# Kernel optimization log

Hardware: AMD Instinct MI355X
Metric: run time of the kernel (lower is better)

## Reference

```python
import jax, jax.numpy as jnp
import numpy as np

N_IM, N_OBJ = 16, 16          # images, objects per image
D_IN = 2048                    # obj_pair_feat_dim
PER_IM = N_OBJ * (N_OBJ + 1) // 2   # obj boxes + union boxes per image
N_BOX = N_IM * PER_IM               # 2176
N_PAIR = N_IM * N_OBJ * (N_OBJ - 1) # is_ex=True -> 2*C(n,2) per image = 3840
NUM_REL = 3


def setup_inputs() -> dict:
    rng = np.random.default_rng(0)
    H, W = 600.0, 800.0
    boxes = np.zeros((N_BOX, 5), np.float32)
    o1i, o2i, ui, imi = [], [], [], []
    for i in range(N_IM):
        off = i * PER_IM
        x1 = rng.uniform(0, W / 2, N_OBJ); y1 = rng.uniform(0, H / 2, N_OBJ)
        bw = rng.uniform(10, W / 2, N_OBJ); bh = rng.uniform(10, H / 2, N_OBJ)
        boxes[off:off + N_OBJ] = np.stack([np.full(N_OBJ, i), x1, y1, x1 + bw, y1 + bh], 1)
        uc = off + N_OBJ
        for a in range(N_OBJ):
            for b in range(a + 1, N_OBJ):
                boxes[uc] = [i, min(x1[a], x1[b]), min(y1[a], y1[b]),
                             max(x1[a] + bw[a], x1[b] + bw[b]), max(y1[a] + bh[a], y1[b] + bh[b])]
                o1i += [off + a, off + b]; o2i += [off + b, off + a]
                ui += [uc, uc]; imi += [i, i]
                uc += 1
    im_info = np.tile(np.array([H, W, 1.0], np.float32), (N_IM, 1))
    key = jax.random.key(0)
    ks = jax.random.split(key, 16)
    lin = lambda k, i, o: jax.random.normal(k, (i, o), jnp.float32) * 0.02
    return dict(
        xs=jax.random.normal(ks[0], (N_PAIR, D_IN), jnp.float32) * 0.1,
        xo=jax.random.normal(ks[1], (N_PAIR, D_IN), jnp.float32) * 0.1,
        xu=jax.random.normal(ks[2], (N_PAIR, D_IN), jnp.float32) * 0.1,
        boxes=jnp.asarray(boxes), im_info=jnp.asarray(im_info),
        o1_idx=jnp.asarray(o1i, jnp.int32), o2_idx=jnp.asarray(o2i, jnp.int32),
        u_idx=jnp.asarray(ui, jnp.int32), img_idx=jnp.asarray(imi, jnp.int32),
        Ws1=lin(ks[3], D_IN, 512), bs1=jnp.zeros(512, jnp.float32),
        Ws2=lin(ks[4], 512, 256), bs2=jnp.zeros(256, jnp.float32),
        Wo1=lin(ks[5], D_IN, 512), bo1=jnp.zeros(512, jnp.float32),
        Wo2=lin(ks[6], 512, 256), bo2=jnp.zeros(256, jnp.float32),
        Wu1=lin(ks[7], D_IN, 512), bu1=jnp.zeros(512, jnp.float32),
        Wu2=lin(ks[8], 512, 256), bu2=jnp.zeros(256, jnp.float32),
        Wc1=lin(ks[9], 256 + 19, 256), bc1=jnp.zeros(256, jnp.float32),
        Wc2=lin(ks[10], 256, NUM_REL), bc2=jnp.zeros(NUM_REL, jnp.float32),
    )


def _mlp(x, W1, b1, W2, b2):
    return jax.nn.relu(jax.nn.relu(x @ W1 + b1) @ W2 + b2)


def _encode_loc(sb, ob, ub, hw):
    # sb/ob/ub: [P,4] (x1,y1,x2,y2); hw: [P,2] (h_i, w_i)
    h_i, w_i = hw[:, 0], hw[:, 1]
    x_s = (sb[:, 0] + sb[:, 2]) / 2.0; y_s = (sb[:, 1] + sb[:, 3]) / 2.0
    w_s = sb[:, 2] - sb[:, 0]; h_s = sb[:, 3] - sb[:, 1]
    x_o = (ob[:, 0] + ob[:, 2]) / 2.0; y_o = (ob[:, 1] + ob[:, 3]) / 2.0
    w_o = ob[:, 2] - ob[:, 0]; h_o = ob[:, 3] - ob[:, 1]
    a_s = w_s * h_s; a_o = w_o * h_o
    a_u = (ub[:, 2] - ub[:, 0]) * (ub[:, 3] - ub[:, 1])
    area = w_i * h_i
    return jnp.stack([
        x_s / w_i, y_s / h_i, (x_s + w_s) / w_i, (y_s + h_s) / h_i, a_s / area,
        x_o / w_i, y_o / h_i, (x_o + w_o) / w_i, (y_o + h_o) / h_i, a_o / area,
        (x_s - x_o) / w_o, (y_s - y_o) / h_o, jnp.log(w_s / w_o), jnp.log(h_s / h_o),
        (x_o - x_s) / w_s, (y_o - y_s) / h_s, jnp.log(w_o / w_s), jnp.log(h_o / h_s),
        a_u / area], axis=1)  # [P,19]


def reference(xs, xo, xu, boxes, im_info, o1_idx, o2_idx, u_idx, img_idx,
              Ws1, bs1, Ws2, bs2, Wo1, bo1, Wo2, bo2, Wu1, bu1, Wu2, bu2,
              Wc1, bc1, Wc2, bc2):
    fs = _mlp(xs, Ws1, bs1, Ws2, bs2)
    fo = _mlp(xo, Wo1, bo1, Wo2, bo2)
    fu = _mlp(xu, Wu1, bu1, Wu2, bu2)
    appear = fu - fo - fs                              # [P,256]
    loc = _encode_loc(boxes[o1_idx, 1:5], boxes[o2_idx, 1:5],
                      boxes[u_idx, 1:5], im_info[img_idx, :2])  # [P,19]
    h = jax.nn.relu(jnp.concatenate([appear, loc], axis=1) @ Wc1 + bc1)
    return h @ Wc2 + bc2                               # [P,num_rel]
```

## Files before the change

### kernel.cpp

```cpp
#include <hip/hip_runtime.h>

#define N_PAIR 3840

typedef short bf16x8 __attribute__((ext_vector_type(8)));
typedef float f32x4 __attribute__((ext_vector_type(4)));

static __device__ __forceinline__ ushort f2bf(float f) {
    uint x = __float_as_uint(f);
    uint r = (x + 0x7FFFu + ((x >> 16) & 1u)) >> 16;
    return (ushort)r;
}
static __device__ __forceinline__ float bf2f(ushort u) {
    return __uint_as_float(((uint)u) << 16);
}

__global__ void transpose_convert(const float* __restrict__ in0,
                                  const float* __restrict__ in1,
                                  const float* __restrict__ in2,
                                  ushort* __restrict__ out,
                                  int K, int N, int Kpad) {
    const float* in = (blockIdx.z == 0) ? in0 : (blockIdx.z == 1 ? in1 : in2);
    ushort* o = out + (size_t)blockIdx.z * N * Kpad;
    __shared__ float tile[64][65];
    int k0 = blockIdx.x * 64, n0 = blockIdx.y * 64;
    int t = threadIdx.x;
    int r = t >> 2, c4 = (t & 3) * 16;
#pragma unroll
    for (int i = 0; i < 16; i++) {
        int k = k0 + r, n = n0 + c4 + i;
        tile[r][c4 + i] = (k < K && n < N) ? in[(size_t)k * N + n] : 0.f;
    }
    __syncthreads();
#pragma unroll
    for (int i = 0; i < 16; i++) {
        int n = n0 + r, k = k0 + c4 + i;
        if (n < N && k < Kpad) o[(size_t)n * Kpad + k] = f2bf(tile[c4 + i][r]);
    }
}

__global__ void transpose_convert2(const float* __restrict__ Ws2,
                                   const float* __restrict__ Wo2,
                                   const float* __restrict__ Wu2,
                                   const float* __restrict__ Wc1,
                                   ushort* __restrict__ W2T,
                                   ushort* __restrict__ WC1T) {
    int z = blockIdx.z;
    const float* in; ushort* o; int K, N, Kpad;
    if (z < 3) {
        in = (z == 0) ? Ws2 : (z == 1 ? Wo2 : Wu2);
        o = W2T + (size_t)z * 256 * 512; K = 512; N = 256; Kpad = 512;
    } else {
        in = Wc1; o = WC1T; K = 275; N = 256; Kpad = 288;
    }
    __shared__ float tile[64][65];
    int k0 = blockIdx.x * 64, n0 = blockIdx.y * 64;
    int t = threadIdx.x;
    int r = t >> 2, c4 = (t & 3) * 16;
#pragma unroll
    for (int i = 0; i < 16; i++) {
        int k = k0 + r, n = n0 + c4 + i;
        tile[r][c4 + i] = (k < K && n < N) ? in[(size_t)k * N + n] : 0.f;
    }
    __syncthreads();
#pragma unroll
    for (int i = 0; i < 16; i++) {
        int n = n0 + r, k = k0 + c4 + i;
        if (n < N && k < Kpad) o[(size_t)n * Kpad + k] = f2bf(tile[c4 + i][r]);
    }
}

__device__ __forceinline__ bf16x8 frag_ld(const ushort* __restrict__ lds, int row, int colbyte) {
    int off = (row << 7) + (colbyte ^ ((row & 7) << 4));
    return *reinterpret_cast<const bf16x8*>(reinterpret_cast<const char*>(lds) + off);
}
__device__ __forceinline__ bf16x8 frag32_ld(const ushort* __restrict__ lds, int row, int colbyte) {
    int off = (row << 6) + (colbyte ^ ((row & 3) << 4));
    return *reinterpret_cast<const bf16x8*>(reinterpret_cast<const char*>(lds) + off);
}

__global__ __launch_bounds__(256) void gemm1(const float* __restrict__ xs,
                                             const float* __restrict__ xo,
                                             const float* __restrict__ xu,
                                             const ushort* __restrict__ w1t,
                                             const float* __restrict__ b_s,
                                             const float* __restrict__ b_o,
                                             const float* __restrict__ b_u,
                                             ushort* __restrict__ h1out) {
    int bid = blockIdx.x;
    int w = (bid & 7) * 90 + (bid >> 3);
    int br = w / 240; int r = w - br * 240;
    int xt = r >> 2, yt = r & 3;

    const float* x = br == 0 ? xs : (br == 1 ? xo : xu);
    const ushort* wt = w1t + (size_t)br * 512 * 2048;
    const float* bias = br == 0 ? b_s : (br == 1 ? b_o : b_u);
    ushort* out = h1out + (size_t)br * 3840 * 512;

    __shared__ ushort As[2][64 * 64];
    __shared__ ushort Bs[2][128 * 64];
    int t = threadIdx.x, lane = t & 63, wid = t >> 6;
    int wr = wid >> 1, wc = wid & 1;
    int m0 = xt * 64, n0 = yt * 128;
    const float* asrc = x + (size_t)m0 * 2048;
    const ushort* bsrc = wt + (size_t)n0 * 2048;

    int ar = t >> 2, ac = (t & 3) * 16;

    float4 pa0[4], pa1[4];
    bf16x8 pb0[4], pb1[4];

#define G1_ISSUE(PA, PB, KT)                                                              \
    {                                                                                     \
        const float4* g = reinterpret_cast<const float4*>(asrc + (size_t)ar * 2048 + (KT) + ac); \
        PA[0] = g[0]; PA[1] = g[1]; PA[2] = g[2]; PA[3] = g[3];                           \
        _Pragma("unroll")                                                                 \
        for (int it = 0; it < 4; it++) {                                                  \
            int e = (it * 256 + t) * 8;                                                   \
            int rr = e >> 6, cc = e & 63;                                                 \
            PB[it] = *reinterpret_cast<const bf16x8*>(bsrc + (size_t)rr * 2048 + (KT) + cc); \
        }                                                                                 \
    }
#define G1_COMMIT(PA, PB, BUF)                                                            \
    {                                                                                     \
        union { bf16x8 v; ushort us[8]; } p0, p1;                                         \
        _Pragma("unroll")                                                                 \
        for (int i = 0; i < 4; i++) {                                                     \
            p0.us[i] = f2bf(PA[0][i]); p0.us[4 + i] = f2bf(PA[1][i]);                     \
            p1.us[i] = f2bf(PA[2][i]); p1.us[4 + i] = f2bf(PA[3][i]);                     \
        }                                                                                 \
        char* ab = reinterpret_cast<char*>(&As[BUF][0]);                                  \
        int off0 = (ar << 7) + ((ac << 1) ^ ((ar & 7) << 4));                             \
        int off1 = (ar << 7) + (((ac + 8) << 1) ^ ((ar & 7) << 4));                       \
        *reinterpret_cast<bf16x8*>(ab + off0) = p0.v;                                     \
        *reinterpret_cast<bf16x8*>(ab + off1) = p1.v;                                     \
        char* bb = reinterpret_cast<char*>(&Bs[BUF][0]);                                  \
        _Pragma("unroll")                                                                 \
        for (int it = 0; it < 4; it++) {                                                  \
            int e = (it * 256 + t) * 8;                                                   \
            int rr = e >> 6, cc = e & 63;                                                 \
            int off = (rr << 7) + ((cc << 1) ^ ((rr & 7) << 4));                          \
            *reinterpret_cast<bf16x8*>(bb + off) = PB[it];                                \
        }                                                                                 \
    }
#define G1_MFMA(BUF)                                                                      \
    _Pragma("unroll")                                                                     \
    for (int kk = 0; kk < 64; kk += 32) {                                                 \
        int cb = (kk + ((lane >> 4) << 3)) << 1;                                          \
        bf16x8 a[2], b[4];                                                                \
        _Pragma("unroll")                                                                 \
        for (int i = 0; i < 2; i++) a[i] = frag_ld(&As[BUF][0], wr * 32 + i * 16 + (lane & 15), cb); \
        _Pragma("unroll")                                                                 \
        for (int f = 0; f < 4; f++) b[f] = frag_ld(&Bs[BUF][0], wc * 64 + f * 16 + (lane & 15), cb); \
        _Pragma("unroll")                                                                 \
        for (int i = 0; i < 2; i++)                                                       \
            _Pragma("unroll")                                                             \
            for (int j = 0; j < 4; j++)                                                   \
                acc[i][j] = __builtin_amdgcn_mfma_f32_16x16x32_bf16(a[i], b[j], acc[i][j], 0, 0, 0); \
    }

    f32x4 acc[2][4] = {};
    G1_ISSUE(pa1, pb1, 0)
    G1_COMMIT(pa1, pb1, 0)
    G1_ISSUE(pa0, pb0, 64)
    __syncthreads();
    for (int kt = 0; kt < 2048; kt += 128) {
        if (kt + 128 < 2048) G1_ISSUE(pa1, pb1, kt + 128)
        G1_MFMA(0)
        if (kt + 64 < 2048) G1_COMMIT(pa0, pb0, 1)
        __syncthreads();
        if (kt + 192 < 2048) G1_ISSUE(pa0, pb0, kt + 192)
        G1_MFMA(1)
        if (kt + 128 < 2048) G1_COMMIT(pa1, pb1, 0)
        __syncthreads();
    }
    int rb = m0 + wr * 32 + ((lane >> 4) << 2);
    int cb0 = n0 + wc * 64 + (lane & 15);
#pragma unroll
    for (int j = 0; j < 4; j++) {
        int col = cb0 + j * 16;
        float bv = bias[col];
#pragma unroll
        for (int i = 0; i < 2; i++)
#pragma unroll
            for (int q = 0; q < 4; q++) {
                int row = rb + i * 16 + q;
                float v = acc[i][j][q] + bv;
                v = v > 0.f ? v : 0.f;
                out[(size_t)row * 512 + col] = f2bf(v);
            }
    }
#undef G1_ISSUE
#undef G1_COMMIT
#undef G1_MFMA
}

__global__ __launch_bounds__(256) void gemm2(const ushort* __restrict__ h1,
                                             const ushort* __restrict__ w2t,
                                             const float* __restrict__ b_s,
                                             const float* __restrict__ b_o,
                                             const float* __restrict__ b_u,
                                             ushort* __restrict__ h2br) {
    int bid = blockIdx.x;
    int w = (bid & 7) * 45 + (bid >> 3);
    int br = w / 120; int r = w - br * 120;
    int xt = r >> 1, yt = r & 1;

    const ushort* A = h1 + (size_t)br * 3840 * 512;
    const ushort* B = w2t + (size_t)br * 256 * 512;
    const float* bias = br == 0 ? b_s : (br == 1 ? b_o : b_u);
    ushort* out = h2br + (size_t)br * 3840 * 256;

    __shared__ ushort As[2][64 * 64];
    __shared__ ushort Bs[2][128 * 64];
    int t = threadIdx.x, lane = t & 63, wid = t >> 6;
    int wr = wid >> 1, wc = wid & 1;
    int m0 = xt * 64, n0 = yt * 128;
    const ushort* asrc = A + (size_t)m0 * 512;
    const ushort* bsrc = B + (size_t)n0 * 512;

    int ar = t >> 2, ac = (t & 3) * 16;
    bf16x8 qa0[2], qa1[2], qb0[4], qb1[4];

#define G2_ISSUE(PA, PB, KT)                                                              \
    {                                                                                     \
        const bf16x8* g = reinterpret_cast<const bf16x8*>(asrc + (size_t)ar * 512 + (KT) + ac); \
        PA[0] = g[0]; PA[1] = g[1];                                                       \
        _Pragma("unroll")                                                                 \
        for (int it = 0; it < 4; it++) {                                                  \
            int e = (it * 256 + t) * 8;                                                   \
            int rr = e >> 6, cc = e & 63;                                                 \
            PB[it] = *reinterpret_cast<const bf16x8*>(bsrc + (size_t)rr * 512 + (KT) + cc); \
        }                                                                                 \
    }
#define G2_COMMIT(PA, PB, BUF)                                                            \
    {                                                                                     \
        char* ab = reinterpret_cast<char*>(&As[BUF][0]);                                  \
        int off0 = (ar << 7) + ((ac << 1) ^ ((ar & 7) << 4));                             \
        int off1 = (ar << 7) + (((ac + 8) << 1) ^ ((ar & 7) << 4));                       \
        *reinterpret_cast<bf16x8*>(ab + off0) = PA[0];                                    \
        *reinterpret_cast<bf16x8*>(ab + off1) = PA[1];                                    \
        char* bb = reinterpret_cast<char*>(&Bs[BUF][0]);                                  \
        _Pragma("unroll")                                                                 \
        for (int it = 0; it < 4; it++) {                                                  \
            int e = (it * 256 + t) * 8;                                                   \
            int rr = e >> 6, cc = e & 63;                                                 \
            int off = (rr << 7) + ((cc << 1) ^ ((rr & 7) << 4));                          \
            *reinterpret_cast<bf16x8*>(bb + off) = PB[it];                                \
        }                                                                                 \
    }
#define G2_MFMA(BUF)                                                                      \
    _Pragma("unroll")                                                                     \
    for (int kk = 0; kk < 64; kk += 32) {                                                 \
        int cb = (kk + ((lane >> 4) << 3)) << 1;                                          \
        bf16x8 a[2], b[4];                                                                \
        _Pragma("unroll")                                                                 \
        for (int i = 0; i < 2; i++) a[i] = frag_ld(&As[BUF][0], wr * 32 + i * 16 + (lane & 15), cb); \
        _Pragma("unroll")                                                                 \
        for (int f = 0; f < 4; f++) b[f] = frag_ld(&Bs[BUF][0], wc * 64 + f * 16 + (lane & 15), cb); \
        _Pragma("unroll")                                                                 \
        for (int i = 0; i < 2; i++)                                                       \
            _Pragma("unroll")                                                             \
            for (int j = 0; j < 4; j++)                                                   \
                acc[i][j] = __builtin_amdgcn_mfma_f32_16x16x32_bf16(a[i], b[j], acc[i][j], 0, 0, 0); \
    }

    f32x4 acc[2][4] = {};
    G2_ISSUE(qa1, qb1, 0)
    G2_COMMIT(qa1, qb1, 0)
    G2_ISSUE(qa0, qb0, 64)
    __syncthreads();
    for (int kt = 0; kt < 512; kt += 128) {
        if (kt + 128 < 512) G2_ISSUE(qa1, qb1, kt + 128)
        G2_MFMA(0)
        if (kt + 64 < 512) G2_COMMIT(qa0, qb0, 1)
        __syncthreads();
        if (kt + 192 < 512) G2_ISSUE(qa0, qb0, kt + 192)
        G2_MFMA(1)
        if (kt + 128 < 512) G2_COMMIT(qa1, qb1, 0)
        __syncthreads();
    }
    int rb = m0 + wr * 32 + ((lane >> 4) << 2);
    int cb0 = n0 + wc * 64 + (lane & 15);
#pragma unroll
    for (int j = 0; j < 4; j++) {
        int col = cb0 + j * 16;
        float bv = bias[col];
#pragma unroll
        for (int i = 0; i < 2; i++)
#pragma unroll
            for (int q = 0; q < 4; q++) {
                int row = rb + i * 16 + q;
                float v = acc[i][j][q] + bv;
                v = v > 0.f ? v : 0.f;
                out[(size_t)row * 256 + col] = f2bf(v);
            }
    }
#undef G2_ISSUE
#undef G2_COMMIT
#undef G2_MFMA
}

__global__ void appear_pack(const ushort* __restrict__ h2br,
                            ushort* __restrict__ hin,
                            const float* __restrict__ boxes,
                            const float* __restrict__ im_info,
                            const int* __restrict__ o1, const int* __restrict__ o2,
                            const int* __restrict__ u, const int* __restrict__ im) {
    int i = blockIdx.x * 256 + threadIdx.x;
    if (i < N_PAIR * 32) {
        int p = i >> 5, ch = (i & 31) * 8;
        const ushort* ps = h2br + (size_t)p * 256 + ch;
        bf16x8 vs = *reinterpret_cast<const bf16x8*>(ps);
        bf16x8 vo = *reinterpret_cast<const bf16x8*>(ps + (size_t)3840 * 256);
        bf16x8 vu = *reinterpret_cast<const bf16x8*>(ps + (size_t)2 * 3840 * 256);
        union { bf16x8 v; ushort us[8]; } r;
#pragma unroll
        for (int j = 0; j < 8; j++)
            r.us[j] = f2bf(bf2f(((ushort)vu[j])) - bf2f(((ushort)vo[j])) - bf2f(((ushort)vs[j])));
        *reinterpret_cast<bf16x8*>(hin + (size_t)p * 288 + ch) = r.v;
    }
    if (blockIdx.x < 15) {
        int p = blockIdx.x * 256 + threadIdx.x;
        const float* sb = boxes + 5 * o1[p] + 1;
        const float* ob = boxes + 5 * o2[p] + 1;
        const float* ub = boxes + 5 * u[p] + 1;
        const float* ii = im_info + 3 * im[p];
        float hi = ii[0], wi = ii[1];
        float x_s = (sb[0] + sb[2]) * 0.5f, y_s = (sb[1] + sb[3]) * 0.5f;
        float w_s = sb[2] - sb[0], h_s = sb[3] - sb[1];
        float x_o = (ob[0] + ob[2]) * 0.5f, y_o = (ob[1] + ob[3]) * 0.5f;
        float w_o = ob[2] - ob[0], h_o = ob[3] - ob[1];
        float a_s = w_s * h_s, a_o = w_o * h_o;
        float a_u = (ub[2] - ub[0]) * (ub[3] - ub[1]);
        float area = wi * hi;
        float f[19];
        f[0] = x_s / wi;            f[1] = y_s / hi;
        f[2] = (x_s + w_s) / wi;    f[3] = (y_s + h_s) / hi;
        f[4] = a_s / area;
        f[5] = x_o / wi;            f[6] = y_o / hi;
        f[7] = (x_o + w_o) / wi;    f[8] = (y_o + h_o) / hi;
        f[9] = a_o / area;
        f[10] = (x_s - x_o) / w_o;  f[11] = (y_s - y_o) / h_o;
        f[12] = logf(w_s / w_o);    f[13] = logf(h_s / h_o);
        f[14] = (x_o - x_s) / w_s;  f[15] = (y_o - y_s) / h_s;
        f[16] = logf(w_o / w_s);    f[17] = logf(h_o / h_s);
        f[18] = a_u / area;
        ushort* row = hin + (size_t)p * 288 + 256;
#pragma unroll
        for (int k = 0; k < 19; k++) row[k] = f2bf(f[k]);
#pragma unroll
        for (int k = 19; k < 32; k++) row[k] = 0;
    }
}

__global__ __launch_bounds__(256) void gemm3(const ushort* __restrict__ hin,
                                             const ushort* __restrict__ wc1t,
                                             const float* __restrict__ bc1,
                                             ushort* __restrict__ h2) {
    __shared__ ushort As[2][64 * 32];
    __shared__ ushort Bs[2][128 * 32];
    int t = threadIdx.x, lane = t & 63, wid = t >> 6;
    int wr = wid >> 1, wc = wid & 1;
    int m0 = blockIdx.x * 64, n0 = blockIdx.y * 128;
    const ushort* asrc = hin + (size_t)m0 * 288;
    const ushort* bsrc = wc1t + (size_t)n0 * 288;

    int ar = t >> 2, ac = (t & 3) * 8;
    bf16x8 pa, pb[2];
    auto issue = [&](int kt) {
        pa = *reinterpret_cast<const bf16x8*>(asrc + (size_t)ar * 288 + kt + ac);
#pragma unroll
        for (int it = 0; it < 2; it++) {
            int e = (it * 256 + t) * 8;
            int rr = e >> 5, cc = e & 31;
            pb[it] = *reinterpret_cast<const bf16x8*>(bsrc + (size_t)rr * 288 + kt + cc);
        }
    };
    auto commit = [&](int buf) {
        char* ab = reinterpret_cast<char*>(&As[buf][0]);
        int off0 = (ar << 6) + ((ac << 1) ^ ((ar & 3) << 4));
        *reinterpret_cast<bf16x8*>(ab + off0) = pa;
        char* bb = reinterpret_cast<char*>(&Bs[buf][0]);
#pragma unroll
        for (int it = 0; it < 2; it++) {
            int e = (it * 256 + t) * 8;
            int rr = e >> 5, cc = e & 31;
            int off = (rr << 6) + ((cc << 1) ^ ((rr & 3) << 4));
            *reinterpret_cast<bf16x8*>(bb + off) = pb[it];
        }
    };

    f32x4 acc[2][4] = {};
    issue(0);
    commit(0);
    __syncthreads();
    int cur = 0;
    for (int kt = 0; kt < 288; kt += 32) {
        int nxt = kt + 32;
        if (nxt < 288) issue(nxt);
        int cb = ((lane >> 4) << 3) << 1;
        bf16x8 a[2], b[4];
#pragma unroll
        for (int i = 0; i < 2; i++) a[i] = frag32_ld(&As[cur][0], wr * 32 + i * 16 + (lane & 15), cb);
#pragma unroll
        for (int f = 0; f < 4; f++) b[f] = frag32_ld(&Bs[cur][0], wc * 64 + f * 16 + (lane & 15), cb);
#pragma unroll
        for (int i = 0; i < 2; i++)
#pragma unroll
            for (int j = 0; j < 4; j++)
                acc[i][j] = __builtin_amdgcn_mfma_f32_16x16x32_bf16(a[i], b[j], acc[i][j], 0, 0, 0);
        if (nxt < 288) commit(cur ^ 1);
        __syncthreads();
        cur ^= 1;
    }
    int rb = m0 + wr * 32 + ((lane >> 4) << 2);
    int cb0 = n0 + wc * 64 + (lane & 15);
#pragma unroll
    for (int j = 0; j < 4; j++) {
        int col = cb0 + j * 16;
        float bv = bc1[col];
#pragma unroll
        for (int i = 0; i < 2; i++)
#pragma unroll
            for (int q = 0; q < 4; q++) {
                int row = rb + i * 16 + q;
                float v = acc[i][j][q] + bv;
                v = v > 0.f ? v : 0.f;
                h2[(size_t)row * 256 + col] = f2bf(v);
            }
    }
}

__global__ void final_fc(const ushort* __restrict__ h2,
                         const float* __restrict__ wc2,
                         const float* __restrict__ bc2,
                         float* __restrict__ out) {
    __shared__ float w[768];
    int t = threadIdx.x;
    for (int i = t; i < 768; i += 256) w[i] = wc2[i];
    __syncthreads();
    int g = t >> 4, l = t & 15;
    int row = blockIdx.x * 16 + g;
    const ushort* hr = h2 + (size_t)row * 256 + l * 16;
    bf16x8 v0 = *reinterpret_cast<const bf16x8*>(hr);
    bf16x8 v1 = *reinterpret_cast<const bf16x8*>(hr + 8);
    float s0 = 0.f, s1 = 0.f, s2 = 0.f;
#pragma unroll
    for (int k = 0; k < 8; k++) {
        float h = bf2f((ushort)v0[k]);
        int c = (l * 16 + k) * 3;
        s0 += h * w[c]; s1 += h * w[c + 1]; s2 += h * w[c + 2];
    }
#pragma unroll
    for (int k = 0; k < 8; k++) {
        float h = bf2f((ushort)v1[k]);
        int c = (l * 16 + 8 + k) * 3;
        s0 += h * w[c]; s1 += h * w[c + 1]; s2 += h * w[c + 2];
    }
#pragma unroll
    for (int m = 1; m < 16; m <<= 1) {
        s0 += __shfl_xor(s0, m);
        s1 += __shfl_xor(s1, m);
        s2 += __shfl_xor(s2, m);
    }
    if (l == 0) {
        out[row * 3 + 0] = s0 + bc2[0];
        out[row * 3 + 1] = s1 + bc2[1];
        out[row * 3 + 2] = s2 + bc2[2];
    }
}

extern "C" void kernel_launch(void* const* d_in, const int* in_sizes, int n_in,
                              void* d_out, int out_size, void* d_ws, size_t ws_size,
                              hipStream_t stream) {
    (void)in_sizes; (void)n_in; (void)out_size; (void)ws_size;
    const float* xs = (const float*)d_in[0];
    const float* xo = (const float*)d_in[1];
    const float* xu = (const float*)d_in[2];
    const float* boxes = (const float*)d_in[3];
    const float* im_info = (const float*)d_in[4];
    const int* o1 = (const int*)d_in[5];
    const int* o2 = (const int*)d_in[6];
    const int* uu = (const int*)d_in[7];
    const int* im = (const int*)d_in[8];
    const float* Ws1 = (const float*)d_in[9];
    const float* bs1 = (const float*)d_in[10];
    const float* Ws2 = (const float*)d_in[11];
    const float* bs2 = (const float*)d_in[12];
    const float* Wo1 = (const float*)d_in[13];
    const float* bo1 = (const float*)d_in[14];
    const float* Wo2 = (const float*)d_in[15];
    const float* bo2 = (const float*)d_in[16];
    const float* Wu1 = (const float*)d_in[17];
    const float* bu1 = (const float*)d_in[18];
    const float* Wu2 = (const float*)d_in[19];
    const float* bu2 = (const float*)d_in[20];
    const float* Wc1 = (const float*)d_in[21];
    const float* bc1 = (const float*)d_in[22];
    const float* Wc2 = (const float*)d_in[23];
    const float* bc2 = (const float*)d_in[24];
    float* out = (float*)d_out;

    ushort* W1T = (ushort*)d_ws;
    ushort* H2BR = W1T;
    ushort* W2T = W1T + (size_t)3 * 512 * 2048;
    ushort* WC1T = W2T + (size_t)3 * 256 * 512;
    ushort* H1 = WC1T + (size_t)256 * 288;
    ushort* HIN = H1 + (size_t)3 * 3840 * 512;
    ushort* H2 = HIN + (size_t)3840 * 288;

    transpose_convert<<<dim3(32, 8, 3), 256, 0, stream>>>(Ws1, Wo1, Wu1, W1T, 2048, 512, 2048);
    transpose_convert2<<<dim3(8, 4, 4), 256, 0, stream>>>(Ws2, Wo2, Wu2, Wc1, W2T, WC1T);
    gemm1<<<720, 256, 0, stream>>>(xs, xo, xu, W1T, bs1, bo1, bu1, H1);
    gemm2<<<360, 256, 0, stream>>>(H1, W2T, bs2, bo2, bu2, H2BR);
    appear_pack<<<480, 256, 0, stream>>>(H2BR, HIN, boxes, im_info, o1, o2, uu, im);
    gemm3<<<dim3(60, 2), 256, 0, stream>>>(HIN, WC1T, bc1, H2);
    final_fc<<<240, 256, 0, stream>>>(H2, Wc2, bc2, out);
}
```

Measured before the change: 97.22 us.

## Retile first-layer GEMM to 128x64 blocks and shorten prefetch distance

```diff
diff --git a/kernel.cpp b/kernel.cpp
--- a/kernel.cpp
+++ b/kernel.cpp
@@ -89,32 +89,33 @@
     int bid = blockIdx.x;
     int w = (bid & 7) * 90 + (bid >> 3);
     int br = w / 240; int r = w - br * 240;
-    int xt = r >> 2, yt = r & 3;
+    int mt = r >> 3, nt = r & 7;
 
     const float* x = br == 0 ? xs : (br == 1 ? xo : xu);
     const ushort* wt = w1t + (size_t)br * 512 * 2048;
     const float* bias = br == 0 ? b_s : (br == 1 ? b_o : b_u);
     ushort* out = h1out + (size_t)br * 3840 * 512;
 
-    __shared__ ushort As[2][64 * 64];
-    __shared__ ushort Bs[2][128 * 64];
+    __shared__ ushort As[2][128 * 64];
+    __shared__ ushort Bs[2][64 * 64];
     int t = threadIdx.x, lane = t & 63, wid = t >> 6;
     int wr = wid >> 1, wc = wid & 1;
-    int m0 = xt * 64, n0 = yt * 128;
+    int m0 = mt * 128, n0 = nt * 64;
     const float* asrc = x + (size_t)m0 * 2048;
     const ushort* bsrc = wt + (size_t)n0 * 2048;
 
-    int ar = t >> 2, ac = (t & 3) * 16;
-
-    float4 pa0[4], pa1[4];
-    bf16x8 pb0[4], pb1[4];
+    int arow = t >> 1, ac0 = (t & 1) * 32;
+
+    float4 pa0[8], pa1[8];
+    bf16x8 pb0[2], pb1[2];
 
 #define G1_ISSUE(PA, PB, KT)                                                              \
     {                                                                                     \
-        const float4* g = reinterpret_cast<const float4*>(asrc + (size_t)ar * 2048 + (KT) + ac); \
-        PA[0] = g[0]; PA[1] = g[1]; PA[2] = g[2]; PA[3] = g[3];                           \
-        _Pragma("unroll")                                                                 \
-        for (int it = 0; it < 4; it++) {                                                  \
+        const float4* g = reinterpret_cast<const float4*>(asrc + (size_t)arow * 2048 + (KT) + ac0); \
+        _Pragma("unroll")                                                                 \
+        for (int i = 0; i < 8; i++) PA[i] = g[i];                                         \
+        _Pragma("unroll")                                                                 \
+        for (int it = 0; it < 2; it++) {                                                  \
             int e = (it * 256 + t) * 8;                                                   \
             int rr = e >> 6, cc = e & 63;                                                 \
             PB[it] = *reinterpret_cast<const bf16x8*>(bsrc + (size_t)rr * 2048 + (KT) + cc); \
@@ -122,20 +123,22 @@
     }
 #define G1_COMMIT(PA, PB, BUF)                                                            \
     {                                                                                     \
-        union { bf16x8 v; ushort us[8]; } p0, p1;                                         \
-        _Pragma("unroll")                                                                 \
-        for (int i = 0; i < 4; i++) {                                                     \
-            p0.us[i] = f2bf(PA[0][i]); p0.us[4 + i] = f2bf(PA[1][i]);                     \
-            p1.us[i] = f2bf(PA[2][i]); p1.us[4 + i] = f2bf(PA[3][i]);                     \
+        char* ab = reinterpret_cast<char*>(&As[BUF][0]);                                  \
+        _Pragma("unroll")                                                                 \
+        for (int j = 0; j < 4; j++) {                                                     \
+            union { bf16x8 v; ushort us[8]; } pk;                                         \
+            _Pragma("unroll")                                                             \
+            for (int i = 0; i < 4; i++) {                                                 \
+                pk.us[i] = f2bf(PA[2 * j][i]);                                            \
+                pk.us[4 + i] = f2bf(PA[2 * j + 1][i]);                                    \
+            }                                                                             \
+            int cj = ac0 + j * 8;                                                         \
+            int off = (arow << 7) + ((cj << 1) ^ ((arow & 7) << 4));                      \
+            *reinterpret_cast<bf16x8*>(ab + off) = pk.v;                                  \
         }                                                                                 \
-        char* ab = reinterpret_cast<char*>(&As[BUF][0]);                                  \
-        int off0 = (ar << 7) + ((ac << 1) ^ ((ar & 7) << 4));                             \
-        int off1 = (ar << 7) + (((ac + 8) << 1) ^ ((ar & 7) << 4));                       \
-        *reinterpret_cast<bf16x8*>(ab + off0) = p0.v;                                     \
-        *reinterpret_cast<bf16x8*>(ab + off1) = p1.v;                                     \
         char* bb = reinterpret_cast<char*>(&Bs[BUF][0]);                                  \
         _Pragma("unroll")                                                                 \
-        for (int it = 0; it < 4; it++) {                                                  \
+        for (int it = 0; it < 2; it++) {                                                  \
             int e = (it * 256 + t) * 8;                                                   \
             int rr = e >> 6, cc = e & 63;                                                 \
             int off = (rr << 7) + ((cc << 1) ^ ((rr & 7) << 4));                          \
@@ -146,41 +149,41 @@
     _Pragma("unroll")                                                                     \
     for (int kk = 0; kk < 64; kk += 32) {                                                 \
         int cb = (kk + ((lane >> 4) << 3)) << 1;                                          \
-        bf16x8 a[2], b[4];                                                                \
-        _Pragma("unroll")                                                                 \
-        for (int i = 0; i < 2; i++) a[i] = frag_ld(&As[BUF][0], wr * 32 + i * 16 + (lane & 15), cb); \
-        _Pragma("unroll")                                                                 \
-        for (int f = 0; f < 4; f++) b[f] = frag_ld(&Bs[BUF][0], wc * 64 + f * 16 + (lane & 15), cb); \
-        _Pragma("unroll")                                                                 \
-        for (int i = 0; i < 2; i++)                                                       \
+        bf16x8 a[4], b[2];                                                                \
+        _Pragma("unroll")                                                                 \
+        for (int i = 0; i < 4; i++) a[i] = frag_ld(&As[BUF][0], wr * 64 + i * 16 + (lane & 15), cb); \
+        _Pragma("unroll")                                                                 \
+        for (int j = 0; j < 2; j++) b[j] = frag_ld(&Bs[BUF][0], wc * 32 + j * 16 + (lane & 15), cb); \
+        _Pragma("unroll")                                                                 \
+        for (int i = 0; i < 4; i++)                                                       \
             _Pragma("unroll")                                                             \
-            for (int j = 0; j < 4; j++)                                                   \
+            for (int j = 0; j < 2; j++)                                                   \
                 acc[i][j] = __builtin_amdgcn_mfma_f32_16x16x32_bf16(a[i], b[j], acc[i][j], 0, 0, 0); \
     }
 
-    f32x4 acc[2][4] = {};
-    G1_ISSUE(pa1, pb1, 0)
-    G1_COMMIT(pa1, pb1, 0)
-    G1_ISSUE(pa0, pb0, 64)
+    f32x4 acc[4][2] = {};
+    G1_ISSUE(pa0, pb0, 0)
+    G1_COMMIT(pa0, pb0, 0)
     __syncthreads();
+    G1_ISSUE(pa1, pb1, 64)
     for (int kt = 0; kt < 2048; kt += 128) {
-        if (kt + 128 < 2048) G1_ISSUE(pa1, pb1, kt + 128)
         G1_MFMA(0)
-        if (kt + 64 < 2048) G1_COMMIT(pa0, pb0, 1)
+        if (kt + 64 < 2048) G1_COMMIT(pa1, pb1, 1)
         __syncthreads();
-        if (kt + 192 < 2048) G1_ISSUE(pa0, pb0, kt + 192)
+        if (kt + 128 < 2048) G1_ISSUE(pa0, pb0, kt + 128)
         G1_MFMA(1)
-        if (kt + 128 < 2048) G1_COMMIT(pa1, pb1, 0)
+        if (kt + 128 < 2048) G1_COMMIT(pa0, pb0, 0)
         __syncthreads();
-    }
-    int rb = m0 + wr * 32 + ((lane >> 4) << 2);
-    int cb0 = n0 + wc * 64 + (lane & 15);
-#pragma unroll
-    for (int j = 0; j < 4; j++) {
+        if (kt + 192 < 2048) G1_ISSUE(pa1, pb1, kt + 192)
+    }
+    int rb = m0 + wr * 64 + ((lane >> 4) << 2);
+    int cb0 = n0 + wc * 32 + (lane & 15);
+#pragma unroll
+    for (int j = 0; j < 2; j++) {
         int col = cb0 + j * 16;
         float bv = bias[col];
 #pragma unroll
-        for (int i = 0; i < 2; i++)
+        for (int i = 0; i < 4; i++)
 #pragma unroll
             for (int q = 0; q < 4; q++) {
                 int row = rb + i * 16 + q;
@@ -265,19 +268,19 @@
     }
 
     f32x4 acc[2][4] = {};
-    G2_ISSUE(qa1, qb1, 0)
-    G2_COMMIT(qa1, qb1, 0)
-    G2_ISSUE(qa0, qb0, 64)
+    G2_ISSUE(qa0, qb0, 0)
+    G2_COMMIT(qa0, qb0, 0)
     __syncthreads();
+    G2_ISSUE(qa1, qb1, 64)
     for (int kt = 0; kt < 512; kt += 128) {
-        if (kt + 128 < 512) G2_ISSUE(qa1, qb1, kt + 128)
         G2_MFMA(0)
-        if (kt + 64 < 512) G2_COMMIT(qa0, qb0, 1)
+        if (kt + 64 < 512) G2_COMMIT(qa1, qb1, 1)
         __syncthreads();
-        if (kt + 192 < 512) G2_ISSUE(qa0, qb0, kt + 192)
+        if (kt + 128 < 512) G2_ISSUE(qa0, qb0, kt + 128)
         G2_MFMA(1)
-        if (kt + 128 < 512) G2_COMMIT(qa1, qb1, 0)
+        if (kt + 128 < 512) G2_COMMIT(qa0, qb0, 0)
         __syncthreads();
+        if (kt + 192 < 512) G2_ISSUE(qa1, qb1, kt + 192)
     }
     int rb = m0 + wr * 32 + ((lane >> 4) << 2);
     int cb0 = n0 + wc * 64 + (lane & 15);
```

After: 161.3 us. 65.9% more time.

## Load bf16 GEMM operands directly into LDS with global_load_lds

Applied to the files above, without the earlier changes.

```diff
diff --git a/kernel.cpp b/kernel.cpp
--- a/kernel.cpp
+++ b/kernel.cpp
@@ -13,6 +13,11 @@
 static __device__ __forceinline__ float bf2f(ushort u) {
     return __uint_as_float(((uint)u) << 16);
 }
+
+#define GLOAD16(GP, LP)                                                        \
+    __builtin_amdgcn_global_load_lds(                                          \
+        (const __attribute__((address_space(1))) void*)(GP),                   \
+        (__attribute__((address_space(3))) void*)(LP), 16, 0, 0)
 
 __global__ void transpose_convert(const float* __restrict__ in0,
                                   const float* __restrict__ in1,
@@ -105,41 +110,36 @@
     const ushort* bsrc = wt + (size_t)n0 * 2048;
 
     int ar = t >> 2, ac = (t & 3) * 16;
-
-    float4 pa0[4], pa1[4];
-    bf16x8 pb0[4], pb1[4];
-
-#define G1_ISSUE(PA, PB, KT)                                                              \
+    float4 pa[4];
+
+#define G1_AISSUE(KT)                                                                     \
     {                                                                                     \
         const float4* g = reinterpret_cast<const float4*>(asrc + (size_t)ar * 2048 + (KT) + ac); \
-        PA[0] = g[0]; PA[1] = g[1]; PA[2] = g[2]; PA[3] = g[3];                           \
-        _Pragma("unroll")                                                                 \
-        for (int it = 0; it < 4; it++) {                                                  \
-            int e = (it * 256 + t) * 8;                                                   \
-            int rr = e >> 6, cc = e & 63;                                                 \
-            PB[it] = *reinterpret_cast<const bf16x8*>(bsrc + (size_t)rr * 2048 + (KT) + cc); \
-        }                                                                                 \
-    }
-#define G1_COMMIT(PA, PB, BUF)                                                            \
+        pa[0] = g[0]; pa[1] = g[1]; pa[2] = g[2]; pa[3] = g[3];                           \
+    }
+#define G1_ACOMMIT(BUF)                                                                   \
     {                                                                                     \
         union { bf16x8 v; ushort us[8]; } p0, p1;                                         \
         _Pragma("unroll")                                                                 \
         for (int i = 0; i < 4; i++) {                                                     \
-            p0.us[i] = f2bf(PA[0][i]); p0.us[4 + i] = f2bf(PA[1][i]);                     \
-            p1.us[i] = f2bf(PA[2][i]); p1.us[4 + i] = f2bf(PA[3][i]);                     \
+            p0.us[i] = f2bf(pa[0][i]); p0.us[4 + i] = f2bf(pa[1][i]);                     \
+            p1.us[i] = f2bf(pa[2][i]); p1.us[4 + i] = f2bf(pa[3][i]);                     \
         }                                                                                 \
         char* ab = reinterpret_cast<char*>(&As[BUF][0]);                                  \
         int off0 = (ar << 7) + ((ac << 1) ^ ((ar & 7) << 4));                             \
         int off1 = (ar << 7) + (((ac + 8) << 1) ^ ((ar & 7) << 4));                       \
         *reinterpret_cast<bf16x8*>(ab + off0) = p0.v;                                     \
         *reinterpret_cast<bf16x8*>(ab + off1) = p1.v;                                     \
-        char* bb = reinterpret_cast<char*>(&Bs[BUF][0]);                                  \
+    }
+#define G1_BGLOAD(BUF, KT)                                                                \
+    {                                                                                     \
         _Pragma("unroll")                                                                 \
         for (int it = 0; it < 4; it++) {                                                  \
-            int e = (it * 256 + t) * 8;                                                   \
-            int rr = e >> 6, cc = e & 63;                                                 \
-            int off = (rr << 7) + ((cc << 1) ^ ((rr & 7) << 4));                          \
-            *reinterpret_cast<bf16x8*>(bb + off) = PB[it];                                \
+            int g = (wid * 4 + it) * 64 + lane;                                           \
+            int rr = g >> 3, cc = g & 7;                                                  \
+            const ushort* gp = bsrc + (size_t)rr * 2048 + (KT) + ((cc ^ (rr & 7)) << 3);  \
+            ushort* lp = &Bs[BUF][g * 8];                                                 \
+            GLOAD16(gp, lp);                                                              \
         }                                                                                 \
     }
 #define G1_MFMA(BUF)                                                                      \
@@ -159,19 +159,20 @@
     }
 
     f32x4 acc[2][4] = {};
-    G1_ISSUE(pa1, pb1, 0)
-    G1_COMMIT(pa1, pb1, 0)
-    G1_ISSUE(pa0, pb0, 64)
+    G1_AISSUE(0)
+    G1_BGLOAD(0, 0)
+    G1_ACOMMIT(0)
     __syncthreads();
-    for (int kt = 0; kt < 2048; kt += 128) {
-        if (kt + 128 < 2048) G1_ISSUE(pa1, pb1, kt + 128)
-        G1_MFMA(0)
-        if (kt + 64 < 2048) G1_COMMIT(pa0, pb0, 1)
+    int cur = 0;
+    for (int kt = 0; kt < 2048; kt += 64) {
+        if (kt + 64 < 2048) {
+            G1_BGLOAD(cur ^ 1, kt + 64)
+            G1_AISSUE(kt + 64)
+        }
+        G1_MFMA(cur)
+        if (kt + 64 < 2048) G1_ACOMMIT(cur ^ 1)
         __syncthreads();
-        if (kt + 192 < 2048) G1_ISSUE(pa0, pb0, kt + 192)
-        G1_MFMA(1)
-        if (kt + 128 < 2048) G1_COMMIT(pa1, pb1, 0)
-        __syncthreads();
+        cur ^= 1;
     }
     int rb = m0 + wr * 32 + ((lane >> 4) << 2);
     int cb0 = n0 + wc * 64 + (lane & 15);
@@ -189,8 +190,9 @@
                 out[(size_t)row * 512 + col] = f2bf(v);
             }
     }
-#undef G1_ISSUE
-#undef G1_COMMIT
+#undef G1_AISSUE
+#undef G1_ACOMMIT
+#undef G1_BGLOAD
 #undef G1_MFMA
 }
 
@@ -218,34 +220,21 @@
     const ushort* asrc = A + (size_t)m0 * 512;
     const ushort* bsrc = B + (size_t)n0 * 512;
 
-    int ar = t >> 2, ac = (t & 3) * 16;
-    bf16x8 qa0[2], qa1[2], qb0[4], qb1[4];
-
-#define G2_ISSUE(PA, PB, KT)                                                              \
+#define G2_GLOADS(BUF, KT)                                                                \
     {                                                                                     \
-        const bf16x8* g = reinterpret_cast<const bf16x8*>(asrc + (size_t)ar * 512 + (KT) + ac); \
-        PA[0] = g[0]; PA[1] = g[1];                                                       \
+        _Pragma("unroll")                                                                 \
+        for (int it = 0; it < 2; it++) {                                                  \
+            int g = (wid * 2 + it) * 64 + lane;                                           \
+            int rr = g >> 3, cc = g & 7;                                                  \
+            const ushort* gp = asrc + (size_t)rr * 512 + (KT) + ((cc ^ (rr & 7)) << 3);   \
+            GLOAD16(gp, &As[BUF][g * 8]);                                                 \
+        }                                                                                 \
         _Pragma("unroll")                                                                 \
         for (int it = 0; it < 4; it++) {                                                  \
-            int e = (it * 256 + t) * 8;                                                   \
-            int rr = e >> 6, cc = e & 63;                                                 \
-            PB[it] = *reinterpret_cast<const bf16x8*>(bsrc + (size_t)rr * 512 + (KT) + cc); \
-        }                                                                                 \
-    }
-#define G2_COMMIT(PA, PB, BUF)                                                            \
-    {                                                                                     \
-        char* ab = reinterpret_cast<char*>(&As[BUF][0]);                                  \
-        int off0 = (ar << 7) + ((ac << 1) ^ ((ar & 7) << 4));                             \
-        int off1 = (ar << 7) + (((ac + 8) << 1) ^ ((ar & 7) << 4));                       \
-        *reinterpret_cast<bf16x8*>(ab + off0) = PA[0];                                    \
-        *reinterpret_cast<bf16x8*>(ab + off1) = PA[1];                                    \
-        char* bb = reinterpret_cast<char*>(&Bs[BUF][0]);                                  \
-        _Pragma("unroll")                                                                 \
-        for (int it = 0; it < 4; it++) {                                                  \
-            int e = (it * 256 + t) * 8;                                                   \
-            int rr = e >> 6, cc = e & 63;                                                 \
-            int off = (rr << 7) + ((cc << 1) ^ ((rr & 7) << 4));                          \
-            *reinterpret_cast<bf16x8*>(bb + off) = PB[it];                                \
+            int g = (wid * 4 + it) * 64 + lane;                                           \
+            int rr = g >> 3, cc = g & 7;                                                  \
+            const ushort* gp = bsrc + (size_t)rr * 512 + (KT) + ((cc ^ (rr & 7)) << 3);   \
+            GLOAD16(gp, &Bs[BUF][g * 8]);                                                 \
         }                                                                                 \
     }
 #define G2_MFMA(BUF)                                                                      \
@@ -265,19 +254,14 @@
     }
 
     f32x4 acc[2][4] = {};
-    G2_ISSUE(qa1, qb1, 0)
-    G2_COMMIT(qa1, qb1, 0)
-    G2_ISSUE(qa0, qb0, 64)
+    G2_GLOADS(0, 0)
     __syncthreads();
-    for (int kt = 0; kt < 512; kt += 128) {
-        if (kt + 128 < 512) G2_ISSUE(qa1, qb1, kt + 128)
-        G2_MFMA(0)
-        if (kt + 64 < 512) G2_COMMIT(qa0, qb0, 1)
+    int cur = 0;
+    for (int kt = 0; kt < 512; kt += 64) {
+        if (kt + 64 < 512) G2_GLOADS(cur ^ 1, kt + 64)
+        G2_MFMA(cur)
         __syncthreads();
-        if (kt + 192 < 512) G2_ISSUE(qa0, qb0, kt + 192)
-        G2_MFMA(1)
-        if (kt + 128 < 512) G2_COMMIT(qa1, qb1, 0)
-        __syncthreads();
+        cur ^= 1;
     }
     int rb = m0 + wr * 32 + ((lane >> 4) << 2);
     int cb0 = n0 + wc * 64 + (lane & 15);
@@ -295,8 +279,7 @@
                 out[(size_t)row * 256 + col] = f2bf(v);
             }
     }
-#undef G2_ISSUE
-#undef G2_COMMIT
+#undef G2_GLOADS
 #undef G2_MFMA
 }
 
```

New measurement: 99.98 us. 2.8% more time.
